# Kernel tuning notes

Hardware: AMD Instinct MI355X
Metric: run time of the kernel (lower is better)

The kernel has to match this reference:

```python
import jax, jax.numpy as jnp
import numpy as np

B, S, D, H = 4, 2048, 768, 12
DH = D // H  # 64


def setup_inputs() -> dict:
    key = jax.random.key(0)
    ks = jax.random.split(key, 7)
    return {
        "sequences": jax.random.normal(ks[0], (B, S, D), dtype=jnp.float32),
        "wq": jax.random.normal(ks[1], (H, DH, DH), dtype=jnp.float32) / np.sqrt(DH),
        "bq": jax.random.normal(ks[2], (H, DH), dtype=jnp.float32) * 0.02,
        "wk": jax.random.normal(ks[3], (H, DH, DH), dtype=jnp.float32) / np.sqrt(DH),
        "bk": jax.random.normal(ks[4], (H, DH), dtype=jnp.float32) * 0.02,
        "wv": jax.random.normal(ks[5], (H, DH, DH), dtype=jnp.float32) / np.sqrt(DH),
        "bv": jax.random.normal(ks[6], (H, DH), dtype=jnp.float32) * 0.02,
    }


def reference(sequences, wq, bq, wk, bk, wv, bv):
    # split channels into heads: [B, S, H, DH]
    xh = sequences.reshape(B, S, H, DH)
    # per-head linear projections (weight applied as x @ W^T + b, matching nn.Linear)
    q = jnp.einsum("bshd,hed->bshe", xh, wq) + bq  # [B,S,H,DH]
    k = jnp.einsum("bshd,hed->bshe", xh, wk) + bk
    v = jnp.einsum("bshd,hed->bshe", xh, wv) + bv
    scale = 1.0 / np.sqrt(DH).astype(np.float32)
    scores = jnp.einsum("bqhd,bkhd->bhqk", q, k) * scale  # [B,H,S,S]
    attn = jax.nn.softmax(scores, axis=-1)
    out = jnp.einsum("bhqk,bkhd->bqhd", attn, v)  # [B,S,H,DH]
    return out.reshape(B, S, D)
```

## Files before the change

### kernel.cpp

```cpp
#include <hip/hip_runtime.h>

#define NB 4
#define NS 2048
#define ND 768
#define NH 12
#define NDH 64
#define XPITCH 72
#define SSCALE 0.18033688011112043f

typedef __bf16 bf16x8 __attribute__((ext_vector_type(8)));
typedef float  f32x4  __attribute__((ext_vector_type(4)));
typedef unsigned int u32;

#define MFMA16(a, b, c) __builtin_amdgcn_mfma_f32_16x16x32_bf16(a, b, c, 0, 0, 0)

__device__ __forceinline__ u32 packbf(float a, float b) {
    u32 ua = __builtin_bit_cast(u32, a) + 0x8000u;
    u32 ub = __builtin_bit_cast(u32, b) + 0x8000u;
    return __builtin_amdgcn_perm(ub, ua, 0x07060302u);
}

__device__ __forceinline__ bf16x8 cvt8(float4 a, float4 b) {
    union { u32 u[4]; bf16x8 v; } r;
    r.u[0] = packbf(a.x, a.y); r.u[1] = packbf(a.z, a.w);
    r.u[2] = packbf(b.x, b.y); r.u[3] = packbf(b.z, b.w);
    return r.v;
}

__device__ __forceinline__ __bf16 f2bf(float f) {
    u32 u = __builtin_bit_cast(u32, f) + 0x8000u;
    unsigned short s = (unsigned short)(u >> 16);
    return __builtin_bit_cast(__bf16, s);
}

__device__ __forceinline__ void gl16(const __bf16* g, __bf16* l) {
    __builtin_amdgcn_global_load_lds(
        (const __attribute__((address_space(1))) unsigned int*)g,
        (__attribute__((address_space(3))) unsigned int*)l,
        16, 0, 0);
}


__global__ __launch_bounds__(256, 4) void proj_kernel(
    const float* __restrict__ x,
    const float* __restrict__ wq, const float* __restrict__ bq,
    const float* __restrict__ wk, const float* __restrict__ bk,
    const float* __restrict__ wv, const float* __restrict__ bv,
    __bf16* __restrict__ qws, __bf16* __restrict__ kws, __bf16* __restrict__ vtws)
{
    const int st = blockIdx.x, h = blockIdx.y, b = blockIdx.z;
    const int s0 = st * 64;
    const int tid = threadIdx.x;

    __shared__ __align__(16) __bf16 Xs[64 * XPITCH];
    __shared__ __align__(16) __bf16 Tv[64 * XPITCH];

    const int r = tid >> 2, f = tid & 3;
    const int lane = tid & 63, w = tid >> 6, col = lane & 15, quad = lane >> 4;

    const size_t wrow = (size_t)(h * NDH + w * 16 + col) * NDH;
    const float* wq0 = wq + wrow + quad * 8;
    const float* wk0 = wk + wrow + quad * 8;
    const float* wv0 = wv + wrow + quad * 8;
    const bf16x8 wqa0 = cvt8(*(const float4*)(wq0),      *(const float4*)(wq0 + 4));
    const bf16x8 wqa1 = cvt8(*(const float4*)(wq0 + 32), *(const float4*)(wq0 + 36));
    const bf16x8 wka0 = cvt8(*(const float4*)(wk0),      *(const float4*)(wk0 + 4));
    const bf16x8 wka1 = cvt8(*(const float4*)(wk0 + 32), *(const float4*)(wk0 + 36));
    const bf16x8 wva0 = cvt8(*(const float4*)(wv0),      *(const float4*)(wv0 + 4));
    const bf16x8 wva1 = cvt8(*(const float4*)(wv0 + 32), *(const float4*)(wv0 + 36));

    float bqs[4], bks[4], bvs[4];
#pragma unroll
    for (int rr = 0; rr < 4; ++rr) {
        const int e = h * NDH + w * 16 + quad * 4 + rr;
        bqs[rr] = bq[e] * SSCALE;
        bks[rr] = bk[e];
        bvs[rr] = bv[e];
    }

    const size_t bh = (size_t)(b * NH + h);

    {
        const float* xrow = x + (size_t)(b * NS + s0 + r) * ND + h * NDH + f * 16;
        const float4 v0 = *(const float4*)(xrow);
        const float4 v1 = *(const float4*)(xrow + 4);
        const float4 v2 = *(const float4*)(xrow + 8);
        const float4 v3 = *(const float4*)(xrow + 12);
        *(bf16x8*)&Xs[r * XPITCH + f * 16]     = cvt8(v0, v1);
        *(bf16x8*)&Xs[r * XPITCH + f * 16 + 8] = cvt8(v2, v3);
    }
    __syncthreads();

    const int e0 = w * 16 + quad * 4;
    const int jj = e0 >> 5;
    const int qa = (e0 >> 3) & 3;
    const int hf = (e0 >> 2) & 1;
    const int Lf = qa * 16 + col;
    const int kt = st >> 1;

#pragma unroll
    for (int nt = 0; nt < 4; ++nt) {
        const bf16x8 xb0 = *(const bf16x8*)&Xs[(nt * 16 + col) * XPITCH + quad * 8];
        const bf16x8 xb1 = *(const bf16x8*)&Xs[(nt * 16 + col) * XPITCH + 32 + quad * 8];
        f32x4 aq = {0.f, 0.f, 0.f, 0.f};
        f32x4 ak = {0.f, 0.f, 0.f, 0.f};
        f32x4 av = {0.f, 0.f, 0.f, 0.f};
        aq = MFMA16(wqa0, xb0, aq); aq = MFMA16(wqa1, xb1, aq);
        ak = MFMA16(wka0, xb0, ak); ak = MFMA16(wka1, xb1, ak);
        av = MFMA16(wva0, xb0, av); av = MFMA16(wva1, xb1, av);

        union { u32 u[2]; uint2 v; } pq, pk;
        pq.u[0] = packbf(fmaf(aq[0], SSCALE, bqs[0]), fmaf(aq[1], SSCALE, bqs[1]));
        pq.u[1] = packbf(fmaf(aq[2], SSCALE, bqs[2]), fmaf(aq[3], SSCALE, bqs[3]));
        pk.u[0] = packbf(ak[0] + bks[0], ak[1] + bks[1]);
        pk.u[1] = packbf(ak[2] + bks[2], ak[3] + bks[3]);

        const int wa = (st & 1) * 2 + (nt >> 1);
        const int mt = nt & 1;
        const size_t kidx = ((((((size_t)bh * 16 + kt) * 4 + wa) * 2 + mt) * 2 + jj) * 64 + Lf) * 8 + hf * 4;
        const size_t qidx = (((((size_t)bh * 32 + st) * 4 + nt) * 2 + jj) * 64 + Lf) * 8 + hf * 4;
        *(uint2*)(kws + kidx) = pk.v;
        *(uint2*)(qws + qidx) = pq.v;

        const int pos = ((nt >> 1) << 5) + ((col >> 2) << 3) + ((nt & 1) << 2) + (col & 3);
#pragma unroll
        for (int rr = 0; rr < 4; ++rr)
            Tv[(w * 16 + quad * 4 + rr) * XPITCH + pos] = f2bf(av[rr] + bvs[rr]);
    }
    __syncthreads();

    {
        const uint4 v0 = *(const uint4*)&Tv[r * XPITCH + f * 16];
        const uint4 v1 = *(const uint4*)&Tv[r * XPITCH + f * 16 + 8];
        const int wv_ = (st & 1) * 2 + (f >> 1);
        const int dtv = r >> 4;
        const int colv = r & 15;
        const int L0 = ((f & 1) * 2 + 0) * 16 + colv;
        const int L1 = ((f & 1) * 2 + 1) * 16 + colv;
        const size_t vbase = (((size_t)bh * 16 + kt) * 4 + wv_) * 4 + dtv;
        *(uint4*)(vtws + (vbase * 64 + L0) * 8) = v0;
        *(uint4*)(vtws + (vbase * 64 + L1) * 8) = v1;
    }
}

__global__ __launch_bounds__(256, 4) void attn_kernel(
    const __bf16* __restrict__ qws, const __bf16* __restrict__ kws,
    const __bf16* __restrict__ vtws, float* __restrict__ out)
{
    const int bid = blockIdx.x;
    const int xcd = bid & 7;
    const int j   = bid >> 3;
    const int g   = xcd * 6 + (j >> 5);
    const int qt  = j & 31;
    const int h   = g % NH;
    const int b   = g / NH;

    const int q0 = qt * 64;
    const int tid = threadIdx.x;

    __shared__ __align__(16) unsigned char smem[33280];
    __bf16* ldsK = (__bf16*)smem;
    __bf16* ldsV = (__bf16*)(smem + 16384);
    float* slab  = (float*)smem;
    float* lbuf  = (float*)(smem + 32768);

    const size_t bh = (size_t)(b * NH + h);
    const int lane = tid & 63, w = tid >> 6, col = lane & 15, quad = lane >> 4;
    const int wq = w >> 1, wk = w & 1;

    bf16x8 qb0[2], qb1[2];
    {
        const __bf16* qp = qws + (size_t)bh * 131072 + (size_t)qt * 4096
                         + wq * 2048 + lane * 8;
#pragma unroll
        for (int nt = 0; nt < 2; ++nt) {
            qb0[nt] = *(const bf16x8*)(qp + nt * 1024);
            qb1[nt] = *(const bf16x8*)(qp + nt * 1024 + 512);
        }
    }

    const __bf16* kg = kws  + (size_t)bh * 131072 + wk * 2048 + lane * 8;
    const __bf16* vg = vtws + (size_t)bh * 131072 + wk * 2048 + lane * 8;
    __bf16* lk  = ldsK + w * 2048;
    __bf16* lv  = ldsV + w * 2048;
    const __bf16* lkr = lk + lane * 8;
    const __bf16* lvr = lv + lane * 8;

    float l[2] = {0.f, 0.f};
    f32x4 o[4][2];
#pragma unroll
    for (int dt = 0; dt < 4; ++dt)
#pragma unroll
        for (int nt = 0; nt < 2; ++nt) o[dt][nt] = (f32x4){0.f, 0.f, 0.f, 0.f};

#pragma unroll
    for (int i = 0; i < 4; ++i) gl16(kg + i * 512, lk + i * 512);
#pragma unroll
    for (int i = 0; i < 4; ++i) gl16(vg + i * 512, lv + i * 512);

    for (int kt = 0; kt < 32; ++kt) {
        asm volatile("s_waitcnt vmcnt(0)" ::: "memory");
        __builtin_amdgcn_sched_barrier(0);

        bf16x8 ka[2][2], va[4];
        ka[0][0] = *(const bf16x8*)(lkr);
        ka[0][1] = *(const bf16x8*)(lkr + 512);
        ka[1][0] = *(const bf16x8*)(lkr + 1024);
        ka[1][1] = *(const bf16x8*)(lkr + 1536);
        va[0] = *(const bf16x8*)(lvr);
        va[1] = *(const bf16x8*)(lvr + 512);
        va[2] = *(const bf16x8*)(lvr + 1024);
        va[3] = *(const bf16x8*)(lvr + 1536);

        asm volatile("s_waitcnt lgkmcnt(0)" ::: "memory");
        __builtin_amdgcn_sched_barrier(0);

        if (kt + 1 < 32) {
            const __bf16* kgn = kg + (size_t)(kt + 1) * 4096;
            const __bf16* vgn = vg + (size_t)(kt + 1) * 4096;
#pragma unroll
            for (int i = 0; i < 4; ++i) gl16(kgn + i * 512, lk + i * 512);
#pragma unroll
            for (int i = 0; i < 4; ++i) gl16(vgn + i * 512, lv + i * 512);
        }

#pragma unroll
        for (int nt = 0; nt < 2; ++nt) {
            f32x4 sA = {0.f, 0.f, 0.f, 0.f};
            f32x4 sB = {0.f, 0.f, 0.f, 0.f};
            sA = MFMA16(ka[0][0], qb0[nt], sA); sA = MFMA16(ka[0][1], qb1[nt], sA);
            sB = MFMA16(ka[1][0], qb0[nt], sB); sB = MFMA16(ka[1][1], qb1[nt], sB);

            const float p0 = __builtin_amdgcn_exp2f(sA[0]);
            const float p1 = __builtin_amdgcn_exp2f(sA[1]);
            const float p2 = __builtin_amdgcn_exp2f(sA[2]);
            const float p3 = __builtin_amdgcn_exp2f(sA[3]);
            const float p4 = __builtin_amdgcn_exp2f(sB[0]);
            const float p5 = __builtin_amdgcn_exp2f(sB[1]);
            const float p6 = __builtin_amdgcn_exp2f(sB[2]);
            const float p7 = __builtin_amdgcn_exp2f(sB[3]);
            l[nt] += ((p0 + p1) + (p2 + p3)) + ((p4 + p5) + (p6 + p7));

            union { u32 u[4]; bf16x8 v; } pb;
            pb.u[0] = packbf(p0, p1);
            pb.u[1] = packbf(p2, p3);
            pb.u[2] = packbf(p4, p5);
            pb.u[3] = packbf(p6, p7);

#pragma unroll
            for (int dt = 0; dt < 4; ++dt)
                o[dt][nt] = MFMA16(va[dt], pb.v, o[dt][nt]);
        }
    }

#pragma unroll
    for (int nt = 0; nt < 2; ++nt) {
        l[nt] += __shfl_xor(l[nt], 16, 64);
        l[nt] += __shfl_xor(l[nt], 32, 64);
    }

    __syncthreads();
    if (quad == 0) {
#pragma unroll
        for (int nt = 0; nt < 2; ++nt)
            lbuf[wk * 64 + wq * 32 + nt * 16 + col] = l[nt];
    }
    __syncthreads();

    float scale[2];
#pragma unroll
    for (int nt = 0; nt < 2; ++nt) {
        const int ri = wq * 32 + nt * 16 + col;
        scale[nt] = 1.0f / (lbuf[ri] + lbuf[64 + ri]);
    }
#pragma unroll
    for (int dt = 0; dt < 4; ++dt)
#pragma unroll
        for (int nt = 0; nt < 2; ++nt) o[dt][nt] *= scale[nt];

    if (wk == 0) {
#pragma unroll
        for (int dt = 0; dt < 4; ++dt)
#pragma unroll
            for (int nt = 0; nt < 2; ++nt)
                *(f32x4*)&slab[(wq * 32 + nt * 16 + col) * 68 + dt * 16 + quad * 4] = o[dt][nt];
    }
    __syncthreads();
    if (wk == 1) {
#pragma unroll
        for (int dt = 0; dt < 4; ++dt)
#pragma unroll
            for (int nt = 0; nt < 2; ++nt) {
                f32x4* p = (f32x4*)&slab[(wq * 32 + nt * 16 + col) * 68 + dt * 16 + quad * 4];
                *p = *p + o[dt][nt];
            }
    }
    __syncthreads();

    const int qr = tid >> 2, fq = tid & 3;
#pragma unroll
    for (int j2 = 0; j2 < 4; ++j2) {
        const f32x4 a = *(const f32x4*)&slab[qr * 68 + fq * 16 + j2 * 4];
        *(f32x4*)&out[(size_t)(b * NS + q0 + qr) * ND + h * NDH + fq * 16 + j2 * 4] = a;
    }
}

extern "C" void kernel_launch(void* const* d_in, const int* in_sizes, int n_in,
                              void* d_out, int out_size, void* d_ws, size_t ws_size,
                              hipStream_t stream) {
    (void)in_sizes; (void)n_in; (void)out_size; (void)ws_size;
    const float* x  = (const float*)d_in[0];
    const float* wq = (const float*)d_in[1];
    const float* bq = (const float*)d_in[2];
    const float* wk = (const float*)d_in[3];
    const float* bk = (const float*)d_in[4];
    const float* wv = (const float*)d_in[5];
    const float* bv = (const float*)d_in[6];
    float* out = (float*)d_out;

    __bf16* qws  = (__bf16*)d_ws;
    __bf16* kws  = qws + (size_t)NB * NH * NS * NDH;
    __bf16* vtws = kws + (size_t)NB * NH * NS * NDH;

    dim3 grid(NS / 64, NH, NB);
    proj_kernel<<<grid, 256, 0, stream>>>(x, wq, bq, wk, bk, wv, bv, qws, kws, vtws);
    attn_kernel<<<dim3(NS / 64 * NH * NB), 256, 0, stream>>>(qws, kws, vtws, out);
}
```

Measured before the change: 171.1 us.

## Load V directly to registers and double-buffer K tiles in LDS

V fragments are now read straight from global memory into registers each iteration instead of being staged through LDS. K is double-buffered across two LDS slots, so the next tile's async copy overlaps the current tile's compute. Finer vmcnt waits let the QK^T and exp work proceed while the V loads are still in flight. This removes the full vmcnt(0) stall at the top of every iteration and halves LDS traffic, but the direct V loads put global latency on the PV path and rely on precise counter accounting being correct.

```diff
diff --git a/kernel.cpp b/kernel.cpp
--- a/kernel.cpp
+++ b/kernel.cpp
@@ -160,7 +160,6 @@
 
     __shared__ __align__(16) unsigned char smem[33280];
     __bf16* ldsK = (__bf16*)smem;
-    __bf16* ldsV = (__bf16*)(smem + 16384);
     float* slab  = (float*)smem;
     float* lbuf  = (float*)(smem + 32768);
 
@@ -181,10 +180,10 @@
 
     const __bf16* kg = kws  + (size_t)bh * 131072 + wk * 2048 + lane * 8;
     const __bf16* vg = vtws + (size_t)bh * 131072 + wk * 2048 + lane * 8;
-    __bf16* lk  = ldsK + w * 2048;
-    __bf16* lv  = ldsV + w * 2048;
-    const __bf16* lkr = lk + lane * 8;
-    const __bf16* lvr = lv + lane * 8;
+    __bf16* lk0 = ldsK + w * 2048;
+    __bf16* lk1 = ldsK + 8192 + w * 2048;
+    const __bf16* lkr0 = lk0 + lane * 8;
+    const __bf16* lkr1 = lk1 + lane * 8;
 
     float l[2] = {0.f, 0.f};
     f32x4 o[4][2];
@@ -193,65 +192,68 @@
 #pragma unroll
         for (int nt = 0; nt < 2; ++nt) o[dt][nt] = (f32x4){0.f, 0.f, 0.f, 0.f};
 
-#pragma unroll
-    for (int i = 0; i < 4; ++i) gl16(kg + i * 512, lk + i * 512);
-#pragma unroll
-    for (int i = 0; i < 4; ++i) gl16(vg + i * 512, lv + i * 512);
-
-    for (int kt = 0; kt < 32; ++kt) {
-        asm volatile("s_waitcnt vmcnt(0)" ::: "memory");
-        __builtin_amdgcn_sched_barrier(0);
-
-        bf16x8 ka[2][2], va[4];
-        ka[0][0] = *(const bf16x8*)(lkr);
-        ka[0][1] = *(const bf16x8*)(lkr + 512);
-        ka[1][0] = *(const bf16x8*)(lkr + 1024);
-        ka[1][1] = *(const bf16x8*)(lkr + 1536);
-        va[0] = *(const bf16x8*)(lvr);
-        va[1] = *(const bf16x8*)(lvr + 512);
-        va[2] = *(const bf16x8*)(lvr + 1024);
-        va[3] = *(const bf16x8*)(lvr + 1536);
-
-        asm volatile("s_waitcnt lgkmcnt(0)" ::: "memory");
-        __builtin_amdgcn_sched_barrier(0);
-
-        if (kt + 1 < 32) {
-            const __bf16* kgn = kg + (size_t)(kt + 1) * 4096;
-            const __bf16* vgn = vg + (size_t)(kt + 1) * 4096;
-#pragma unroll
-            for (int i = 0; i < 4; ++i) gl16(kgn + i * 512, lk + i * 512);
-#pragma unroll
-            for (int i = 0; i < 4; ++i) gl16(vgn + i * 512, lv + i * 512);
-        }
-
-#pragma unroll
-        for (int nt = 0; nt < 2; ++nt) {
-            f32x4 sA = {0.f, 0.f, 0.f, 0.f};
-            f32x4 sB = {0.f, 0.f, 0.f, 0.f};
-            sA = MFMA16(ka[0][0], qb0[nt], sA); sA = MFMA16(ka[0][1], qb1[nt], sA);
-            sB = MFMA16(ka[1][0], qb0[nt], sB); sB = MFMA16(ka[1][1], qb1[nt], sB);
-
-            const float p0 = __builtin_amdgcn_exp2f(sA[0]);
-            const float p1 = __builtin_amdgcn_exp2f(sA[1]);
-            const float p2 = __builtin_amdgcn_exp2f(sA[2]);
-            const float p3 = __builtin_amdgcn_exp2f(sA[3]);
-            const float p4 = __builtin_amdgcn_exp2f(sB[0]);
-            const float p5 = __builtin_amdgcn_exp2f(sB[1]);
-            const float p6 = __builtin_amdgcn_exp2f(sB[2]);
-            const float p7 = __builtin_amdgcn_exp2f(sB[3]);
-            l[nt] += ((p0 + p1) + (p2 + p3)) + ((p4 + p5) + (p6 + p7));
-
-            union { u32 u[4]; bf16x8 v; } pb;
-            pb.u[0] = packbf(p0, p1);
-            pb.u[1] = packbf(p2, p3);
-            pb.u[2] = packbf(p4, p5);
-            pb.u[3] = packbf(p6, p7);
-
-#pragma unroll
-            for (int dt = 0; dt < 4; ++dt)
-                o[dt][nt] = MFMA16(va[dt], pb.v, o[dt][nt]);
-        }
-    }
+#define ATTN_ITER(ktv, LKRD, LKN, DMA_C, PV_LAST) do {                        \
+        const __bf16* _vp = vg + (size_t)(ktv) * 4096;                        \
+        const bf16x8 va0 = *(const bf16x8*)(_vp);                             \
+        const bf16x8 va1 = *(const bf16x8*)(_vp + 512);                       \
+        const bf16x8 va2 = *(const bf16x8*)(_vp + 1024);                      \
+        const bf16x8 va3 = *(const bf16x8*)(_vp + 1536);                      \
+        __builtin_amdgcn_sched_barrier(0);                                    \
+        asm volatile("s_waitcnt vmcnt(4)" ::: "memory");                      \
+        __builtin_amdgcn_sched_barrier(0);                                    \
+        const bf16x8 ka00 = *(const bf16x8*)(LKRD);                           \
+        const bf16x8 ka01 = *(const bf16x8*)(LKRD + 512);                     \
+        const bf16x8 ka10 = *(const bf16x8*)(LKRD + 1024);                    \
+        const bf16x8 ka11 = *(const bf16x8*)(LKRD + 1536);                    \
+        if (DMA_C) {                                                          \
+            const __bf16* _kn = kg + (size_t)((ktv) + 1) * 4096;              \
+            gl16(_kn,        LKN);        gl16(_kn + 512,  LKN + 512);        \
+            gl16(_kn + 1024, LKN + 1024); gl16(_kn + 1536, LKN + 1536);       \
+        }                                                                     \
+        union { u32 u[4]; bf16x8 v; } pb[2];                                  \
+        _Pragma("unroll")                                                     \
+        for (int nt = 0; nt < 2; ++nt) {                                      \
+            f32x4 sA = {0.f, 0.f, 0.f, 0.f};                                  \
+            f32x4 sB = {0.f, 0.f, 0.f, 0.f};                                  \
+            sA = MFMA16(ka00, qb0[nt], sA); sA = MFMA16(ka01, qb1[nt], sA);   \
+            sB = MFMA16(ka10, qb0[nt], sB); sB = MFMA16(ka11, qb1[nt], sB);   \
+            const float p0 = __builtin_amdgcn_exp2f(sA[0]);                   \
+            const float p1 = __builtin_amdgcn_exp2f(sA[1]);                   \
+            const float p2 = __builtin_amdgcn_exp2f(sA[2]);                   \
+            const float p3 = __builtin_amdgcn_exp2f(sA[3]);                   \
+            const float p4 = __builtin_amdgcn_exp2f(sB[0]);                   \
+            const float p5 = __builtin_amdgcn_exp2f(sB[1]);                   \
+            const float p6 = __builtin_amdgcn_exp2f(sB[2]);                   \
+            const float p7 = __builtin_amdgcn_exp2f(sB[3]);                   \
+            l[nt] += ((p0 + p1) + (p2 + p3)) + ((p4 + p5) + (p6 + p7));       \
+            pb[nt].u[0] = packbf(p0, p1);                                     \
+            pb[nt].u[1] = packbf(p2, p3);                                     \
+            pb[nt].u[2] = packbf(p4, p5);                                     \
+            pb[nt].u[3] = packbf(p6, p7);                                     \
+        }                                                                     \
+        __builtin_amdgcn_sched_barrier(0);                                    \
+        if (PV_LAST) { asm volatile("s_waitcnt vmcnt(0)" ::: "memory"); }     \
+        else         { asm volatile("s_waitcnt vmcnt(4)" ::: "memory"); }     \
+        __builtin_amdgcn_sched_barrier(0);                                    \
+        _Pragma("unroll")                                                     \
+        for (int nt = 0; nt < 2; ++nt) {                                      \
+            o[0][nt] = MFMA16(va0, pb[nt].v, o[0][nt]);                       \
+            o[1][nt] = MFMA16(va1, pb[nt].v, o[1][nt]);                       \
+            o[2][nt] = MFMA16(va2, pb[nt].v, o[2][nt]);                       \
+            o[3][nt] = MFMA16(va3, pb[nt].v, o[3][nt]);                       \
+        }                                                                     \
+    } while (0)
+
+    gl16(kg,        lk0);        gl16(kg + 512,  lk0 + 512);
+    gl16(kg + 1024, lk0 + 1024); gl16(kg + 1536, lk0 + 1536);
+
+    for (int kt2 = 0; kt2 < 30; kt2 += 2) {
+        ATTN_ITER(kt2,     lkr0, lk1, true, false);
+        ATTN_ITER(kt2 + 1, lkr1, lk0, true, false);
+    }
+    ATTN_ITER(30, lkr0, lk1, true,  false);
+    ATTN_ITER(31, lkr1, lk0, false, true);
+#undef ATTN_ITER
 
 #pragma unroll
     for (int nt = 0; nt < 2; ++nt) {
```

After: 162.5 us. 5.0% less time.
